# Optimization experiments

Hardware: AMD Instinct MI355X
Metric: run time of the kernel (lower is better)

The kernel has to match this reference:

```python
import jax, jax.numpy as jnp
import numpy as np

N_NODES = 100000
N_EDGES = 1600000
IN_FEATS = 128
OUT_FEATS = 64


def setup_inputs() -> dict:
    key = jax.random.key(0)
    k1, k2, k3, k4 = jax.random.split(key, 4)
    feat = jax.random.normal(k1, (N_NODES, IN_FEATS), dtype=jnp.float32)
    W = jax.random.normal(k2, (IN_FEATS, OUT_FEATS), dtype=jnp.float32) * (1.0 / np.sqrt(IN_FEATS))
    src = jax.random.randint(k3, (N_EDGES,), 0, N_NODES, dtype=jnp.int64)
    dst = jax.random.randint(k4, (N_EDGES,), 0, N_NODES, dtype=jnp.int64)
    return {"feat": feat, "W": W, "src": src, "dst": dst}


def reference(feat, W, src, dst):
    # Linear projection (bias=False): homogeneous graph -> shared fc
    ft = feat @ W  # [N, out]

    # per-edge dot-product score: e_ij = <ft[src], ft[dst]>
    a = jnp.sum(ft[src] * ft[dst], axis=-1)  # [E]

    # edge softmax segmented by destination node (numerically stable)
    neg_inf = jnp.finfo(a.dtype).min
    m = jax.ops.segment_max(a, dst, num_segments=N_NODES)  # [N]
    m = jnp.where(m == neg_inf, 0.0, m)  # guard zero-in-degree nodes
    e = jnp.exp(a - m[dst])  # [E]
    s = jax.ops.segment_sum(e, dst, num_segments=N_NODES)  # [N]
    s = jnp.where(s == 0.0, 1.0, s)
    sa = e / s[dst]  # [E]

    # weighted scatter-sum aggregation: out[i] = sum_{j in N(i)} sa_ij * ft[j]
    rst = jax.ops.segment_sum(ft[src] * sa[:, None], dst, num_segments=N_NODES)
    return rst
```

## Files before the change

kernel.cpp:

```cpp
#include <hip/hip_runtime.h>
#include <hip/hip_fp16.h>
#include <math.h>

#define N_NODES 100000
#define N_EDGES 1600000
#define IN_F    128
#define OUT_F   64
#define K_BKT     196
#define BKT_SHIFT 9
#define BKT_NODES 512
#define BKT_CAP   10240
#define CHUNK     4096
#define PBLKS     ((N_EDGES + CHUNK - 1) / CHUNK)
#define LTILES    (N_NODES / 16)
#define LBLKS     ((LTILES + 3) / 4)

typedef _Float16 half8 __attribute__((ext_vector_type(8)));
typedef float    f32x4 __attribute__((ext_vector_type(4)));


__global__ __launch_bounds__(256) void partition_linear_kernel(const int* __restrict__ src,
                                                               const int* __restrict__ dst,
                                                               unsigned* __restrict__ staging,
                                                               int* __restrict__ pcnt,
                                                               int* __restrict__ pbase,
                                                               const float* __restrict__ feat,
                                                               const float* __restrict__ W,
                                                               __half* __restrict__ fth) {
    __shared__ int hist[256], lbase[256], sc[256];
    __shared__ unsigned sval[CHUNK];
    int t = threadIdx.x;
    if (blockIdx.x < PBLKS) {
        hist[t] = 0;
        __syncthreads();
        int beg = blockIdx.x * CHUNK;
        int end = min(beg + CHUNK, N_EDGES);
        for (int i = beg + t; i < end; i += 256)
            atomicAdd(&hist[dst[i] >> BKT_SHIFT], 1);
        __syncthreads();
        int v = hist[t];
        sc[t] = v;
        __syncthreads();
        for (int off = 1; off < 256; off <<= 1) {
            int add = (t >= off) ? sc[t - off] : 0;
            __syncthreads();
            sc[t] += add;
            __syncthreads();
        }
        int lb = sc[t] - v;
        lbase[t] = lb;
        pcnt[blockIdx.x * 256 + t]  = v;
        pbase[blockIdx.x * 256 + t] = lb;
        hist[t] = 0;
        __syncthreads();
        for (int i = beg + t; i < end; i += 256) {
            int s = src[i], d = dst[i];
            int b = d >> BKT_SHIFT;
            int r = atomicAdd(&hist[b], 1);
            sval[lbase[b] + r] = (unsigned)s | ((unsigned)(d & (BKT_NODES - 1)) << 17);
        }
        __syncthreads();
        int n = end - beg;
        for (int p = t; p < n; p += 256)
            staging[(size_t)blockIdx.x * CHUNK + p] = sval[p];
        return;
    }
    int gwave = (blockIdx.x - PBLKS) * 4 + (t >> 6);
    if (gwave >= LTILES) return;
    int lane = t & 63;
    int m = lane & 15, kg = lane >> 4;
    int r0 = gwave * 16;

    half8 fb[4][4];
#pragma unroll
    for (int kb = 0; kb < 4; ++kb)
#pragma unroll
        for (int nb = 0; nb < 4; ++nb) {
            const float* wp = W + (size_t)(kb * 32 + kg * 8) * OUT_F + nb * 16 + m;
#pragma unroll
            for (int j = 0; j < 8; ++j)
                fb[kb][nb][j] = (_Float16)wp[j * OUT_F];
        }

    f32x4 acc[4];
#pragma unroll
    for (int nb = 0; nb < 4; ++nb) acc[nb] = (f32x4){0.f, 0.f, 0.f, 0.f};

#pragma unroll
    for (int kb = 0; kb < 4; ++kb) {
        const float4* ap = (const float4*)(feat + (size_t)(r0 + m) * IN_F + kb * 32 + kg * 8);
        float4 a0 = ap[0], a1 = ap[1];
        half8 fa = {(_Float16)a0.x, (_Float16)a0.y, (_Float16)a0.z, (_Float16)a0.w,
                    (_Float16)a1.x, (_Float16)a1.y, (_Float16)a1.z, (_Float16)a1.w};
#pragma unroll
        for (int nb = 0; nb < 4; ++nb)
            acc[nb] = __builtin_amdgcn_mfma_f32_16x16x32_f16(fa, fb[kb][nb], acc[nb], 0, 0, 0);
    }
#pragma unroll
    for (int nb = 0; nb < 4; ++nb)
#pragma unroll
        for (int i = 0; i < 4; ++i)
            fth[(size_t)(r0 + kg * 4 + i) * OUT_F + nb * 16 + m] = __float2half_rn(acc[nb][i]);
}

__global__ __launch_bounds__(1024) void place_kernel(const unsigned* __restrict__ staging,
                                                     const int* __restrict__ pcnt,
                                                     const int* __restrict__ pbase,
                                                     int* __restrict__ row_beg,
                                                     int* __restrict__ row_end,
                                                     int* __restrict__ edge_src) {
    __shared__ unsigned sbuf[BKT_CAP];
    __shared__ int exo[PBLKS];
    __shared__ int pbs[PBLKS];
    __shared__ int s512[512];
    __shared__ int cnt[BKT_NODES], lcur[BKT_NODES];
    __shared__ int ntot;
    int t = threadIdx.x;
    int b = blockIdx.x;

    int d = 0;
    if (t < PBLKS) { d = pcnt[t * 256 + b]; pbs[t] = pbase[t * 256 + b]; }
    if (t < 512) { s512[t] = (t < PBLKS) ? d : 0; cnt[t] = 0; }
    __syncthreads();
    for (int off = 1; off < 512; off <<= 1) {
        int add = (t >= off && t < 512) ? s512[t - off] : 0;
        __syncthreads();
        if (t < 512) s512[t] += add;
        __syncthreads();
    }
    if (t < PBLKS) exo[t] = s512[t] - d;
    if (t == PBLKS - 1) ntot = s512[t];
    __syncthreads();
    int n = ntot;

    for (int i = t; i < n; i += 1024) {
        int lo = 0, hi = PBLKS - 1;
        while (lo < hi) {
            int mid = (lo + hi + 1) >> 1;
            if (exo[mid] <= i) lo = mid; else hi = mid - 1;
        }
        unsigned u = staging[(size_t)lo * CHUNK + pbs[lo] + (i - exo[lo])];
        sbuf[i] = u;
        atomicAdd(&cnt[u >> 17], 1);
    }
    __syncthreads();
    int v = (t < 512) ? cnt[t] : 0;
    if (t < 512) s512[t] = v;
    __syncthreads();
    for (int off = 1; off < 512; off <<= 1) {
        int add = (t >= off && t < 512) ? s512[t - off] : 0;
        __syncthreads();
        if (t < 512) s512[t] += add;
        __syncthreads();
    }
    if (t < 512) {
        int b0 = b * BKT_CAP + s512[t] - v;
        lcur[t] = b0;
        int node = b * BKT_NODES + t;
        if (node < N_NODES) { row_beg[node] = b0; row_end[node] = b0 + v; }
    }
    __syncthreads();
    for (int i = t; i < n; i += 1024) {
        unsigned u = sbuf[i];
        int pos = atomicAdd(&lcur[u >> 17], 1);
        edge_src[pos] = (int)(u & 0x1FFFFu);
    }
}

__global__ __launch_bounds__(256) void fused_node_kernel(const __half* __restrict__ fth,
                                                         const int* __restrict__ row_beg,
                                                         const int* __restrict__ row_end,
                                                         const int* __restrict__ edge_src,
                                                         float* __restrict__ out) {
    const float LOG2E = 1.44269504088896340736f;
    int wave = (blockIdx.x * 256 + threadIdx.x) >> 6;
    int lane = threadIdx.x & 63;
    if (wave >= N_NODES) return;
    int q = lane >> 4, ql = lane & 15;

    int beg = row_beg[wave];
    int end = row_end[wave];

    float2 rd = *(const float2*)(fth + (size_t)wave * OUT_F + 4 * ql);
    __half2 d01 = *(__half2*)&rd.x, d23 = *(__half2*)&rd.y;
    float fd0 = __half2float(d01.x) * LOG2E, fd1 = __half2float(d01.y) * LOG2E;
    float fd2 = __half2float(d23.x) * LOG2E, fd3 = __half2float(d23.y) * LOG2E;

    float m = -1e30f, l = 0.f;
    float a0 = 0.f, a1 = 0.f, a2 = 0.f, a3 = 0.f;

    for (int i = beg; i < end; i += 16) {
        int e0 = i + q, e1 = e0 + 4, e2 = e0 + 8, e3 = e0 + 12;
        bool u0 = e0 < end, u1 = e1 < end, u2 = e2 < end, u3 = e3 < end;
        int s0 = edge_src[u0 ? e0 : beg];
        int s1 = edge_src[u1 ? e1 : beg];
        int s2 = edge_src[u2 ? e2 : beg];
        int s3 = edge_src[u3 ? e3 : beg];
        float2 r0 = *(const float2*)(fth + (size_t)s0 * OUT_F + 4 * ql);
        float2 r1 = *(const float2*)(fth + (size_t)s1 * OUT_F + 4 * ql);
        float2 r2 = *(const float2*)(fth + (size_t)s2 * OUT_F + 4 * ql);
        float2 r3 = *(const float2*)(fth + (size_t)s3 * OUT_F + 4 * ql);
        __half2 A01 = *(__half2*)&r0.x, A23 = *(__half2*)&r0.y;
        __half2 B01 = *(__half2*)&r1.x, B23 = *(__half2*)&r1.y;
        __half2 C01 = *(__half2*)&r2.x, C23 = *(__half2*)&r2.y;
        __half2 D01 = *(__half2*)&r3.x, D23 = *(__half2*)&r3.y;
        float vA0 = __half2float(A01.x), vA1 = __half2float(A01.y);
        float vA2 = __half2float(A23.x), vA3 = __half2float(A23.y);
        float vB0 = __half2float(B01.x), vB1 = __half2float(B01.y);
        float vB2 = __half2float(B23.x), vB3 = __half2float(B23.y);
        float vC0 = __half2float(C01.x), vC1 = __half2float(C01.y);
        float vC2 = __half2float(C23.x), vC3 = __half2float(C23.y);
        float vD0 = __half2float(D01.x), vD1 = __half2float(D01.y);
        float vD2 = __half2float(D23.x), vD3 = __half2float(D23.y);

        float p0 = vA0 * fd0 + vA1 * fd1 + vA2 * fd2 + vA3 * fd3;
        float p1 = vB0 * fd0 + vB1 * fd1 + vB2 * fd2 + vB3 * fd3;
        float p2 = vC0 * fd0 + vC1 * fd1 + vC2 * fd2 + vC3 * fd3;
        float p3 = vD0 * fd0 + vD1 * fd1 + vD2 * fd2 + vD3 * fd3;
#pragma unroll
        for (int dd = 1; dd < 16; dd <<= 1) {
            p0 += __shfl_xor(p0, dd);
            p1 += __shfl_xor(p1, dd);
            p2 += __shfl_xor(p2, dd);
            p3 += __shfl_xor(p3, dd);
        }
        if (!u0) p0 = -1e30f;
        if (!u1) p1 = -1e30f;
        if (!u2) p2 = -1e30f;
        if (!u3) p3 = -1e30f;
        float nm = fmaxf(fmaxf(fmaxf(p0, p1), fmaxf(p2, p3)), m);
        float alpha = exp2f(m - nm);
        float w0 = exp2f(p0 - nm), w1 = exp2f(p1 - nm);
        float w2 = exp2f(p2 - nm), w3 = exp2f(p3 - nm);
        l = l * alpha + ((w0 + w1) + (w2 + w3));
        a0 = a0 * alpha + (w0 * vA0 + w1 * vB0) + (w2 * vC0 + w3 * vD0);
        a1 = a1 * alpha + (w0 * vA1 + w1 * vB1) + (w2 * vC1 + w3 * vD1);
        a2 = a2 * alpha + (w0 * vA2 + w1 * vB2) + (w2 * vC2 + w3 * vD2);
        a3 = a3 * alpha + (w0 * vA3 + w1 * vB3) + (w2 * vC3 + w3 * vD3);
        m = nm;
    }

#pragma unroll
    for (int dd = 16; dd <= 32; dd <<= 1) {
        float m2 = __shfl_xor(m, dd), l2 = __shfl_xor(l, dd);
        float b0 = __shfl_xor(a0, dd), b1 = __shfl_xor(a1, dd);
        float b2 = __shfl_xor(a2, dd), b3 = __shfl_xor(a3, dd);
        float M = fmaxf(m, m2);
        float e1 = exp2f(m - M), e2 = exp2f(m2 - M);
        l = l * e1 + l2 * e2;
        a0 = a0 * e1 + b0 * e2;
        a1 = a1 * e1 + b1 * e2;
        a2 = a2 * e1 + b2 * e2;
        a3 = a3 * e1 + b3 * e2;
        m = M;
    }
    if (q == 0) {
        float inv = (l > 0.f) ? 1.f / l : 0.f;
        *(float4*)(out + (size_t)wave * OUT_F + 4 * ql) =
            make_float4(a0 * inv, a1 * inv, a2 * inv, a3 * inv);
    }
}

extern "C" void kernel_launch(void* const* d_in, const int* in_sizes, int n_in,
                              void* d_out, int out_size, void* d_ws, size_t ws_size,
                              hipStream_t stream) {
    const float* feat = (const float*)d_in[0];
    const float* W    = (const float*)d_in[1];
    const int*   src  = (const int*)d_in[2];
    const int*   dst  = (const int*)d_in[3];
    float* out = (float*)d_out;

    __half*   fth      = (__half*)d_ws;
    unsigned* staging  = (unsigned*)((int*)d_ws + (size_t)N_NODES * OUT_F / 2);
    int*      edge_src = (int*)(staging + (size_t)PBLKS * CHUNK);
    int*      pcnt     = edge_src + (size_t)K_BKT * BKT_CAP;
    int*      pbase    = pcnt + PBLKS * 256;
    int*      row_beg  = pbase + PBLKS * 256;
    int*      row_end  = row_beg + N_NODES;

    partition_linear_kernel<<<PBLKS + LBLKS, 256, 0, stream>>>(src, dst, staging, pcnt, pbase,
                                                               feat, W, fth);
    place_kernel<<<K_BKT, 1024, 0, stream>>>(staging, pcnt, pbase, row_beg, row_end, edge_src);
    fused_node_kernel<<<(N_NODES * 64) / 256, 256, 0, stream>>>(fth, row_beg, row_end, edge_src, out);
}
```

Measured before the change: 195.0 us.

## Use packed fp16 dot2 and DPP reductions in edge loop; simplify staging gather

The per-edge score and the weighted accumulation in the fused node kernel now use packed fp16 dot2 instructions, and the 16-lane shuffle reductions use DPP row operations in place of ds_swizzle/bpermute shuffles. The place kernel drops the per-element binary search over partition offsets and copies each staging segment with one wave per segment, then counts in a separate pass. These changes aim to cut VALU and LDS instruction count in the gather-bound loop and remove binary-search overhead. The cost is an extra pass over shared memory, and softmax weights rounded to fp16 with round-toward-zero, which loses some precision.

```diff
diff --git a/kernel.cpp b/kernel.cpp
--- a/kernel.cpp
+++ b/kernel.cpp
@@ -16,7 +16,29 @@
 #define LBLKS     ((LTILES + 3) / 4)
 
 typedef _Float16 half8 __attribute__((ext_vector_type(8)));
+typedef _Float16 h2 __attribute__((ext_vector_type(2)));
+typedef _Float16 h4 __attribute__((ext_vector_type(4)));
+typedef __fp16   q2v __attribute__((ext_vector_type(2)));
 typedef float    f32x4 __attribute__((ext_vector_type(4)));
+
+__device__ __forceinline__ float fdot2f(h2 a, h2 b, float c) {
+#if __has_builtin(__builtin_amdgcn_fdot2)
+    return __builtin_amdgcn_fdot2(__builtin_bit_cast(q2v, a), __builtin_bit_cast(q2v, b), c, false);
+#else
+    return (float)a[0] * (float)b[0] + (float)a[1] * (float)b[1] + c;
+#endif
+}
+
+#if __has_builtin(__builtin_amdgcn_update_dpp)
+#define DPP_ADD(x, ctrl)                                                                  \
+    (x) += __builtin_bit_cast(float, __builtin_amdgcn_update_dpp(                         \
+               0, __builtin_bit_cast(int, (x)), (ctrl), 0xF, 0xF, true))
+#define REDUCE16(x) do { DPP_ADD(x, 0xB1); DPP_ADD(x, 0x4E); \
+                         DPP_ADD(x, 0x141); DPP_ADD(x, 0x140); } while (0)
+#else
+#define REDUCE16(x) do { x += __shfl_xor(x, 1); x += __shfl_xor(x, 2); \
+                         x += __shfl_xor(x, 4); x += __shfl_xor(x, 8); } while (0)
+#endif
 
 
 __global__ __launch_bounds__(256) void partition_linear_kernel(const int* __restrict__ src,
@@ -112,6 +134,7 @@
     __shared__ unsigned sbuf[BKT_CAP];
     __shared__ int exo[PBLKS];
     __shared__ int pbs[PBLKS];
+    __shared__ int scnt[PBLKS];
     __shared__ int s512[512];
     __shared__ int cnt[BKT_NODES], lcur[BKT_NODES];
     __shared__ int ntot;
@@ -119,7 +142,7 @@
     int b = blockIdx.x;
 
     int d = 0;
-    if (t < PBLKS) { d = pcnt[t * 256 + b]; pbs[t] = pbase[t * 256 + b]; }
+    if (t < PBLKS) { d = pcnt[t * 256 + b]; pbs[t] = pbase[t * 256 + b]; scnt[t] = d; }
     if (t < 512) { s512[t] = (t < PBLKS) ? d : 0; cnt[t] = 0; }
     __syncthreads();
     for (int off = 1; off < 512; off <<= 1) {
@@ -133,16 +156,18 @@
     __syncthreads();
     int n = ntot;
 
-    for (int i = t; i < n; i += 1024) {
-        int lo = 0, hi = PBLKS - 1;
-        while (lo < hi) {
-            int mid = (lo + hi + 1) >> 1;
-            if (exo[mid] <= i) lo = mid; else hi = mid - 1;
+    {
+        int wid = t >> 6, ln = t & 63;
+        for (int s = wid; s < PBLKS; s += 16) {
+            int c = scnt[s], eo = exo[s];
+            size_t gb = (size_t)s * CHUNK + pbs[s];
+            for (int j = ln; j < c; j += 64)
+                sbuf[eo + j] = staging[gb + j];
         }
-        unsigned u = staging[(size_t)lo * CHUNK + pbs[lo] + (i - exo[lo])];
-        sbuf[i] = u;
-        atomicAdd(&cnt[u >> 17], 1);
-    }
+    }
+    __syncthreads();
+    for (int i = t; i < n; i += 1024)
+        atomicAdd(&cnt[sbuf[i] >> 17], 1);
     __syncthreads();
     int v = (t < 512) ? cnt[t] : 0;
     if (t < 512) s512[t] = v;
@@ -181,10 +206,10 @@
     int beg = row_beg[wave];
     int end = row_end[wave];
 
-    float2 rd = *(const float2*)(fth + (size_t)wave * OUT_F + 4 * ql);
-    __half2 d01 = *(__half2*)&rd.x, d23 = *(__half2*)&rd.y;
-    float fd0 = __half2float(d01.x) * LOG2E, fd1 = __half2float(d01.y) * LOG2E;
-    float fd2 = __half2float(d23.x) * LOG2E, fd3 = __half2float(d23.y) * LOG2E;
+    const _Float16* fh = (const _Float16*)fth;
+    h4 rdv = *(const h4*)(fh + (size_t)wave * OUT_F + 4 * ql);
+    h2 dlo = __builtin_shufflevector(rdv, rdv, 0, 1);
+    h2 dhi = __builtin_shufflevector(rdv, rdv, 2, 3);
 
     float m = -1e30f, l = 0.f;
     float a0 = 0.f, a1 = 0.f, a2 = 0.f, a3 = 0.f;
@@ -196,47 +221,48 @@
         int s1 = edge_src[u1 ? e1 : beg];
         int s2 = edge_src[u2 ? e2 : beg];
         int s3 = edge_src[u3 ? e3 : beg];
-        float2 r0 = *(const float2*)(fth + (size_t)s0 * OUT_F + 4 * ql);
-        float2 r1 = *(const float2*)(fth + (size_t)s1 * OUT_F + 4 * ql);
-        float2 r2 = *(const float2*)(fth + (size_t)s2 * OUT_F + 4 * ql);
-        float2 r3 = *(const float2*)(fth + (size_t)s3 * OUT_F + 4 * ql);
-        __half2 A01 = *(__half2*)&r0.x, A23 = *(__half2*)&r0.y;
-        __half2 B01 = *(__half2*)&r1.x, B23 = *(__half2*)&r1.y;
-        __half2 C01 = *(__half2*)&r2.x, C23 = *(__half2*)&r2.y;
-        __half2 D01 = *(__half2*)&r3.x, D23 = *(__half2*)&r3.y;
-        float vA0 = __half2float(A01.x), vA1 = __half2float(A01.y);
-        float vA2 = __half2float(A23.x), vA3 = __half2float(A23.y);
-        float vB0 = __half2float(B01.x), vB1 = __half2float(B01.y);
-        float vB2 = __half2float(B23.x), vB3 = __half2float(B23.y);
-        float vC0 = __half2float(C01.x), vC1 = __half2float(C01.y);
-        float vC2 = __half2float(C23.x), vC3 = __half2float(C23.y);
-        float vD0 = __half2float(D01.x), vD1 = __half2float(D01.y);
-        float vD2 = __half2float(D23.x), vD3 = __half2float(D23.y);
-
-        float p0 = vA0 * fd0 + vA1 * fd1 + vA2 * fd2 + vA3 * fd3;
-        float p1 = vB0 * fd0 + vB1 * fd1 + vB2 * fd2 + vB3 * fd3;
-        float p2 = vC0 * fd0 + vC1 * fd1 + vC2 * fd2 + vC3 * fd3;
-        float p3 = vD0 * fd0 + vD1 * fd1 + vD2 * fd2 + vD3 * fd3;
-#pragma unroll
-        for (int dd = 1; dd < 16; dd <<= 1) {
-            p0 += __shfl_xor(p0, dd);
-            p1 += __shfl_xor(p1, dd);
-            p2 += __shfl_xor(p2, dd);
-            p3 += __shfl_xor(p3, dd);
-        }
-        if (!u0) p0 = -1e30f;
-        if (!u1) p1 = -1e30f;
-        if (!u2) p2 = -1e30f;
-        if (!u3) p3 = -1e30f;
+        h4 rA = *(const h4*)(fh + (size_t)s0 * OUT_F + 4 * ql);
+        h4 rB = *(const h4*)(fh + (size_t)s1 * OUT_F + 4 * ql);
+        h4 rC = *(const h4*)(fh + (size_t)s2 * OUT_F + 4 * ql);
+        h4 rD = *(const h4*)(fh + (size_t)s3 * OUT_F + 4 * ql);
+
+        float p0 = fdot2f(__builtin_shufflevector(rA, rA, 0, 1), dlo,
+                   fdot2f(__builtin_shufflevector(rA, rA, 2, 3), dhi, 0.f));
+        float p1 = fdot2f(__builtin_shufflevector(rB, rB, 0, 1), dlo,
+                   fdot2f(__builtin_shufflevector(rB, rB, 2, 3), dhi, 0.f));
+        float p2 = fdot2f(__builtin_shufflevector(rC, rC, 0, 1), dlo,
+                   fdot2f(__builtin_shufflevector(rC, rC, 2, 3), dhi, 0.f));
+        float p3 = fdot2f(__builtin_shufflevector(rD, rD, 0, 1), dlo,
+                   fdot2f(__builtin_shufflevector(rD, rD, 2, 3), dhi, 0.f));
+        REDUCE16(p0);
+        REDUCE16(p1);
+        REDUCE16(p2);
+        REDUCE16(p3);
+        p0 = u0 ? p0 * LOG2E : -1e30f;
+        p1 = u1 ? p1 * LOG2E : -1e30f;
+        p2 = u2 ? p2 * LOG2E : -1e30f;
+        p3 = u3 ? p3 * LOG2E : -1e30f;
+
         float nm = fmaxf(fmaxf(fmaxf(p0, p1), fmaxf(p2, p3)), m);
         float alpha = exp2f(m - nm);
         float w0 = exp2f(p0 - nm), w1 = exp2f(p1 - nm);
         float w2 = exp2f(p2 - nm), w3 = exp2f(p3 - nm);
         l = l * alpha + ((w0 + w1) + (w2 + w3));
-        a0 = a0 * alpha + (w0 * vA0 + w1 * vB0) + (w2 * vC0 + w3 * vD0);
-        a1 = a1 * alpha + (w0 * vA1 + w1 * vB1) + (w2 * vC1 + w3 * vD1);
-        a2 = a2 * alpha + (w0 * vA2 + w1 * vB2) + (w2 * vC2 + w3 * vD2);
-        a3 = a3 * alpha + (w0 * vA3 + w1 * vB3) + (w2 * vC3 + w3 * vD3);
+#if __has_builtin(__builtin_amdgcn_cvt_pkrtz)
+        h2 wlo = __builtin_bit_cast(h2, __builtin_amdgcn_cvt_pkrtz(w0, w1));
+        h2 whi = __builtin_bit_cast(h2, __builtin_amdgcn_cvt_pkrtz(w2, w3));
+#else
+        h2 wlo = {(_Float16)w0, (_Float16)w1};
+        h2 whi = {(_Float16)w2, (_Float16)w3};
+#endif
+        h2 cab0 = {rA[0], rB[0]}, ccd0 = {rC[0], rD[0]};
+        h2 cab1 = {rA[1], rB[1]}, ccd1 = {rC[1], rD[1]};
+        h2 cab2 = {rA[2], rB[2]}, ccd2 = {rC[2], rD[2]};
+        h2 cab3 = {rA[3], rB[3]}, ccd3 = {rC[3], rD[3]};
+        a0 = fdot2f(wlo, cab0, fdot2f(whi, ccd0, a0 * alpha));
+        a1 = fdot2f(wlo, cab1, fdot2f(whi, ccd1, a1 * alpha));
+        a2 = fdot2f(wlo, cab2, fdot2f(whi, ccd2, a2 * alpha));
+        a3 = fdot2f(wlo, cab3, fdot2f(whi, ccd3, a3 * alpha));
         m = nm;
     }
 
```

Result: faster. 188.8 us (-3.2%).
